# Kernel optimization log

Measured on AMD Instinct MI355X. Metric: run time of the kernel, lower is better.

## Reference

```python
import jax, jax.numpy as jnp
import numpy as np

N_NODES = 100000
N_EDGES = 1600000
IN_DIM = 128
HID_DIM = 128
OUT_DIM = 64
NUM_GRAPHS = 64


def setup_inputs() -> dict:
    key = jax.random.key(0)
    k = jax.random.split(key, 8)
    x = jax.random.normal(k[0], (N_NODES, IN_DIM), dtype=jnp.float32)
    edge_index = jax.random.randint(k[1], (2, N_EDGES), 0, N_NODES, dtype=jnp.int64)
    batch = jnp.sort(jax.random.randint(k[2], (N_NODES,), 0, NUM_GRAPHS, dtype=jnp.int64))
    # glorot-ish init for GCN weights, zero bias (PyG default)
    W1 = jax.random.normal(k[3], (IN_DIM, HID_DIM), dtype=jnp.float32) / np.sqrt(IN_DIM)
    b1 = jnp.zeros((HID_DIM,), dtype=jnp.float32)
    W2 = jax.random.normal(k[4], (HID_DIM, OUT_DIM), dtype=jnp.float32) / np.sqrt(HID_DIM)
    b2 = jnp.zeros((OUT_DIM,), dtype=jnp.float32)
    return {"x": x, "edge_index": edge_index, "batch": batch,
            "W1": W1, "b1": b1, "W2": W2, "b2": b2}


def _gcn_conv(x, W, b, src, dst, norm, n_nodes):
    # x' = scatter_add_{dst}(norm * (xW)[src]) + b   (self-loops already in src/dst)
    h = x @ W                              # [N, D_out]
    msg = norm[:, None] * h[src]           # [E+N, D_out] gather + scale
    out = jax.ops.segment_sum(msg, dst, num_segments=n_nodes)
    return out + b


def _gcn_norm(src, dst, n_nodes):
    # symmetric normalization with self-loops: deg^-1/2[src] * deg^-1/2[dst]
    deg = jax.ops.segment_sum(jnp.ones_like(dst, dtype=jnp.float32), dst,
                              num_segments=n_nodes)
    dinv = jnp.where(deg > 0, jax.lax.rsqrt(deg), 0.0)
    return dinv[src] * dinv[dst]


def reference(x, edge_index, batch, W1, b1, W2, b2):
    n = x.shape[0]
    loops = jnp.arange(n, dtype=edge_index.dtype)
    src = jnp.concatenate([edge_index[0], loops])
    dst = jnp.concatenate([edge_index[1], loops])
    norm = _gcn_norm(src, dst, n)

    h = jax.nn.relu(_gcn_conv(x, W1, b1, src, dst, norm, n))
    h = jax.nn.relu(_gcn_conv(h, W2, b2, src, dst, norm, n))

    # global mean pool per graph
    sums = jax.ops.segment_sum(h, batch, num_segments=NUM_GRAPHS)
    cnts = jax.ops.segment_sum(jnp.ones((n,), dtype=h.dtype), batch,
                               num_segments=NUM_GRAPHS)
    return sums / jnp.maximum(cnts, 1.0)[:, None]
```

## Files before the change

kernel.cpp:

```cpp
#include <hip/hip_runtime.h>

typedef unsigned short ushort_t;
typedef unsigned int uint_t;
typedef __attribute__((ext_vector_type(8))) short bf16x8;
typedef __attribute__((ext_vector_type(4))) float f32x4;

__device__ inline ushort_t bf16_rne(float f) {
    uint_t u = __float_as_uint(f);
    return (ushort_t)((u + 0x7FFFu + ((u >> 16) & 1u)) >> 16);
}

__device__ inline uint_t pack2(float lo, float hi) {
    return (uint_t)bf16_rne(lo) | ((uint_t)bf16_rne(hi) << 16);
}

__device__ inline void acc8(uint4 v, float* a) {
    a[0] += __uint_as_float(v.x << 16);
    a[1] += __uint_as_float(v.x & 0xFFFF0000u);
    a[2] += __uint_as_float(v.y << 16);
    a[3] += __uint_as_float(v.y & 0xFFFF0000u);
    a[4] += __uint_as_float(v.z << 16);
    a[5] += __uint_as_float(v.z & 0xFFFF0000u);
    a[6] += __uint_as_float(v.w << 16);
    a[7] += __uint_as_float(v.w & 0xFFFF0000u);
}

__device__ inline void set8(uint4 v, float* a) {
    a[0] = __uint_as_float(v.x << 16);
    a[1] = __uint_as_float(v.x & 0xFFFF0000u);
    a[2] = __uint_as_float(v.y << 16);
    a[3] = __uint_as_float(v.y & 0xFFFF0000u);
    a[4] = __uint_as_float(v.z << 16);
    a[5] = __uint_as_float(v.z & 0xFFFF0000u);
    a[6] = __uint_as_float(v.w << 16);
    a[7] = __uint_as_float(v.w & 0xFFFF0000u);
}


#define BSH 8
#define NBMAX 512
#define EPB 4096

__global__ __launch_bounds__(256) void k_bhist(const int* __restrict__ dst,
                                               int* __restrict__ bcnt, int E, int nb) {
    __shared__ int h[NBMAX];
    const int tid = threadIdx.x;
    for (int i = tid; i < NBMAX; i += 256) h[i] = 0;
    __syncthreads();
    const int e0 = blockIdx.x * EPB;
    for (int i = tid; i < EPB; i += 256) {
        int e = e0 + i;
        if (e < E) atomicAdd(&h[dst[e] >> BSH], 1);
    }
    __syncthreads();
    for (int i = tid; i < nb; i += 256)
        if (h[i]) atomicAdd(&bcnt[i], h[i]);
}

__global__ __launch_bounds__(512) void k_bscan(const int* __restrict__ bcnt,
                                               int* __restrict__ boff,
                                               int* __restrict__ bcur, int nb) {
    __shared__ int a[NBMAX];
    const int t = threadIdx.x;
    int v = (t < nb) ? bcnt[t] : 0;
    a[t] = v;
    __syncthreads();
    for (int off = 1; off < NBMAX; off <<= 1) {
        int x = (t >= off) ? a[t - off] : 0;
        __syncthreads();
        a[t] += x;
        __syncthreads();
    }
    if (t < nb) {
        int excl = a[t] - v;
        boff[t] = excl;
        bcur[t] = excl;
    }
}

__global__ __launch_bounds__(256) void k_bscatter(const int* __restrict__ src,
                                                  const int* __restrict__ dst,
                                                  int* __restrict__ bcur,
                                                  uint_t* __restrict__ pairs, int E, int nb) {
    __shared__ int h[NBMAX];
    __shared__ int base[NBMAX];
    const int tid = threadIdx.x;
    for (int i = tid; i < NBMAX; i += 256) h[i] = 0;
    __syncthreads();
    const int e0 = blockIdx.x * EPB;
    for (int i = tid; i < EPB; i += 256) {
        int e = e0 + i;
        if (e < E) atomicAdd(&h[dst[e] >> BSH], 1);
    }
    __syncthreads();
    for (int b = tid; b < nb; b += 256) {
        int c = h[b];
        base[b] = c ? atomicAdd(&bcur[b], c) : 0;
        h[b] = 0;
    }
    __syncthreads();
    for (int i = tid; i < EPB; i += 256) {
        int e = e0 + i;
        if (e < E) {
            int s = src[e], d = dst[e];
            int bk = d >> BSH;
            int off = atomicAdd(&h[bk], 1);
            pairs[base[bk] + off] = (uint_t)s | ((uint_t)(d & 255) << 24);
        }
    }
}

__global__ __launch_bounds__(256) void k_bcsr(const uint_t* __restrict__ pairs,
                                              const int* __restrict__ boff,
                                              const int* __restrict__ bcurEnd,
                                              int* __restrict__ rowptr,
                                              int* __restrict__ rowend,
                                              float* __restrict__ dinv,
                                              int* __restrict__ csr, int n) {
    __shared__ int deg[256], sc[256], cur[256];
    const int t = threadIdx.x;
    const int b = blockIdx.x;
    const int beg = boff[b], end = bcurEnd[b];
    deg[t] = 0;
    __syncthreads();
    for (int i = beg + t; i < end; i += 256) {
        uint_t p = pairs[i];
        atomicAdd(&deg[p >> 24], 1);
    }
    __syncthreads();
    int dv = deg[t];
    sc[t] = dv;
    __syncthreads();
    for (int off = 1; off < 256; off <<= 1) {
        int x = (t >= off) ? sc[t - off] : 0;
        __syncthreads();
        sc[t] += x;
        __syncthreads();
    }
    int excl = sc[t] - dv;
    cur[t] = excl;
    int d = (b << BSH) + t;
    if (d < n) {
        int r = beg + excl;
        rowptr[d] = r;
        rowend[d] = r + dv;
        dinv[d] = rsqrtf((float)dv + 1.0f);
    }
    __syncthreads();
    for (int i = beg + t; i < end; i += 256) {
        uint_t p = pairs[i];
        int off = atomicAdd(&cur[p >> 24], 1);
        csr[beg + off] = (int)(p & 0xFFFFFFu);
    }
}


__global__ __launch_bounds__(256) void k_prep_w(const float* __restrict__ W1,
                                                const float* __restrict__ W2,
                                                ushort_t* __restrict__ Wt1,
                                                ushort_t* __restrict__ Wt2) {
    int idx = blockIdx.x * 256 + threadIdx.x;
    if (idx < 16384) {
        int k = idx >> 7, c = idx & 127;
        Wt1[c * 128 + k] = bf16_rne(W1[idx]);
    } else if (idx < 24576) {
        int j = idx - 16384;
        int k = j >> 6, c = j & 63;
        Wt2[c * 128 + k] = bf16_rne(W2[j]);
    }
}


template <int DOUT, bool IN_BF16>
__global__ __launch_bounds__(256) void k_gemm_mfma(const void* __restrict__ Xv,
                                                   const ushort_t* __restrict__ Wt,
                                                   const float* __restrict__ dinv,
                                                   ushort_t* __restrict__ G, int n) {
    constexpr int KP = 136;
    constexpr int NW = DOUT / 2;
    constexpr int NT = NW / 16;
    __shared__ ushort_t Xs[128 * KP];
    __shared__ ushort_t Ws[DOUT * KP];

    const int tid = threadIdx.x;
    const int row0 = blockIdx.x * 128;

    if (!IN_BF16) {
        const float* X = (const float*)Xv;
#pragma unroll
        for (int i = 0; i < 16; i++) {
            int idx = tid * 4 + i * 1024;
            int r = idx >> 7, k = idx & 127;
            int gr = row0 + r;
            float4 v = make_float4(0.f, 0.f, 0.f, 0.f);
            if (gr < n) v = *(const float4*)&X[(size_t)gr * 128 + k];
            ushort4 o;
            o.x = bf16_rne(v.x); o.y = bf16_rne(v.y);
            o.z = bf16_rne(v.z); o.w = bf16_rne(v.w);
            *(ushort4*)&Xs[r * KP + k] = o;
        }
    } else {
        const ushort_t* X = (const ushort_t*)Xv;
#pragma unroll
        for (int i = 0; i < 8; i++) {
            int idx = tid * 8 + i * 2048;
            int r = idx >> 7, k = idx & 127;
            int gr = row0 + r;
            uint4 v = make_uint4(0u, 0u, 0u, 0u);
            if (gr < n) v = *(const uint4*)&X[(size_t)gr * 128 + k];
            *(uint4*)&Xs[r * KP + k] = v;
        }
    }
    constexpr int WI = (DOUT * 128) / 2048;
#pragma unroll
    for (int i = 0; i < WI; i++) {
        int idx = tid * 8 + i * 2048;
        int r = idx >> 7, k = idx & 127;
        *(uint4*)&Ws[r * KP + k] = *(const uint4*)&Wt[idx];
    }
    __syncthreads();

    const int lane = tid & 63;
    const int wid = tid >> 6;
    const int wm = wid & 1, wn = wid >> 1;
    const int lr = lane & 15, kg = lane >> 4;

    f32x4 acc[4][NT];
#pragma unroll
    for (int mi = 0; mi < 4; mi++)
#pragma unroll
        for (int ni = 0; ni < NT; ni++)
#pragma unroll
            for (int q = 0; q < 4; q++) acc[mi][ni][q] = 0.f;

    const ushort_t* xb = &Xs[(wm * 64 + lr) * KP + kg * 8];
    const ushort_t* wb = &Ws[(wn * NW + lr) * KP + kg * 8];

#pragma unroll
    for (int ks = 0; ks < 4; ks++) {
        bf16x8 a[4], b[NT];
#pragma unroll
        for (int mi = 0; mi < 4; mi++)
            a[mi] = *(const bf16x8*)&xb[mi * 16 * KP + ks * 32];
#pragma unroll
        for (int ni = 0; ni < NT; ni++)
            b[ni] = *(const bf16x8*)&wb[ni * 16 * KP + ks * 32];
#pragma unroll
        for (int mi = 0; mi < 4; mi++)
#pragma unroll
            for (int ni = 0; ni < NT; ni++)
                acc[mi][ni] = __builtin_amdgcn_mfma_f32_16x16x32_bf16(
                    a[mi], b[ni], acc[mi][ni], 0, 0, 0);
    }

#pragma unroll
    for (int mi = 0; mi < 4; mi++) {
        int r0 = row0 + wm * 64 + mi * 16 + kg * 4;
#pragma unroll
        for (int r = 0; r < 4; r++) {
            int gr = r0 + r;
            if (gr < n) {
                float s = dinv[gr];
#pragma unroll
                for (int ni = 0; ni < NT; ni++) {
                    int c = wn * NW + ni * 16 + lr;
                    G[(size_t)gr * DOUT + c] = bf16_rne(s * acc[mi][ni][r]);
                }
            }
        }
    }
}


__global__ __launch_bounds__(256) void k_gather128(const int* __restrict__ rowptr,
                                                   const int* __restrict__ rowend,
                                                   const int* __restrict__ csr,
                                                   const ushort_t* __restrict__ G,
                                                   const float* __restrict__ dinv,
                                                   const float* __restrict__ b,
                                                   ushort_t* __restrict__ H, int n) {
    const int g = blockIdx.x * 16 + (threadIdx.x >> 4);
    const int lane = threadIdx.x & 15;
    const int koff = lane * 8;
    if (g >= n) return;
    const int beg = rowptr[g], end = rowend[g];

    float a[8];
    set8(*(const uint4*)&G[(size_t)g * 128 + koff], a);
    int e = beg;
    for (; e + 7 < end; e += 8) {
        int s[8];
#pragma unroll
        for (int j = 0; j < 8; j++) s[j] = csr[e + j];
        uint4 v[8];
#pragma unroll
        for (int j = 0; j < 8; j++)
            v[j] = *(const uint4*)&G[(size_t)s[j] * 128 + koff];
#pragma unroll
        for (int j = 0; j < 8; j++) acc8(v[j], a);
    }
    for (; e + 1 < end; e += 2) {
        int s0 = csr[e], s1 = csr[e + 1];
        uint4 v0 = *(const uint4*)&G[(size_t)s0 * 128 + koff];
        uint4 v1 = *(const uint4*)&G[(size_t)s1 * 128 + koff];
        acc8(v0, a); acc8(v1, a);
    }
    if (e < end) {
        int s0 = csr[e];
        acc8(*(const uint4*)&G[(size_t)s0 * 128 + koff], a);
    }
    const float di = dinv[g];
    float4 bb0 = *(const float4*)&b[koff];
    float4 bb1 = *(const float4*)&b[koff + 4];
    uint4 ov;
    ov.x = pack2(fmaxf(di * a[0] + bb0.x, 0.f), fmaxf(di * a[1] + bb0.y, 0.f));
    ov.y = pack2(fmaxf(di * a[2] + bb0.z, 0.f), fmaxf(di * a[3] + bb0.w, 0.f));
    ov.z = pack2(fmaxf(di * a[4] + bb1.x, 0.f), fmaxf(di * a[5] + bb1.y, 0.f));
    ov.w = pack2(fmaxf(di * a[6] + bb1.z, 0.f), fmaxf(di * a[7] + bb1.w, 0.f));
    *(uint4*)&H[(size_t)g * 128 + koff] = ov;
}


__global__ __launch_bounds__(256) void k_gather64_pool(const int* __restrict__ rowptr,
                                                       const int* __restrict__ rowend,
                                                       const int* __restrict__ csr,
                                                       const ushort_t* __restrict__ G,
                                                       const float* __restrict__ dinv,
                                                       const float* __restrict__ b,
                                                       const int* __restrict__ batch,
                                                       float* __restrict__ pool, int n) {
    __shared__ float po[32][72];
    __shared__ int pg[32];
    const int grp = threadIdx.x >> 3;
    const int lane = threadIdx.x & 7;
    const int g = blockIdx.x * 32 + grp;
    const int koff = lane * 8;

    float o8[8] = {0.f, 0.f, 0.f, 0.f, 0.f, 0.f, 0.f, 0.f};
    if (g < n) {
        float a[8];
        set8(*(const uint4*)&G[(size_t)g * 64 + koff], a);
        int e = rowptr[g];
        const int end = rowend[g];
        for (; e + 7 < end; e += 8) {
            int s[8];
#pragma unroll
            for (int j = 0; j < 8; j++) s[j] = csr[e + j];
            uint4 v[8];
#pragma unroll
            for (int j = 0; j < 8; j++)
                v[j] = *(const uint4*)&G[(size_t)s[j] * 64 + koff];
#pragma unroll
            for (int j = 0; j < 8; j++) acc8(v[j], a);
        }
        for (; e + 1 < end; e += 2) {
            int s0 = csr[e], s1 = csr[e + 1];
            uint4 v0 = *(const uint4*)&G[(size_t)s0 * 64 + koff];
            uint4 v1 = *(const uint4*)&G[(size_t)s1 * 64 + koff];
            acc8(v0, a); acc8(v1, a);
        }
        if (e < end) {
            int s0 = csr[e];
            acc8(*(const uint4*)&G[(size_t)s0 * 64 + koff], a);
        }
        const float di = dinv[g];
        float4 bb0 = *(const float4*)&b[koff];
        float4 bb1 = *(const float4*)&b[koff + 4];
        o8[0] = fmaxf(di * a[0] + bb0.x, 0.f);
        o8[1] = fmaxf(di * a[1] + bb0.y, 0.f);
        o8[2] = fmaxf(di * a[2] + bb0.z, 0.f);
        o8[3] = fmaxf(di * a[3] + bb0.w, 0.f);
        o8[4] = fmaxf(di * a[4] + bb1.x, 0.f);
        o8[5] = fmaxf(di * a[5] + bb1.y, 0.f);
        o8[6] = fmaxf(di * a[6] + bb1.z, 0.f);
        o8[7] = fmaxf(di * a[7] + bb1.w, 0.f);
    }
    if (lane == 0) pg[grp] = (g < n) ? batch[g] : -1;
    *(float4*)&po[grp][koff] = make_float4(o8[0], o8[1], o8[2], o8[3]);
    *(float4*)&po[grp][koff + 4] = make_float4(o8[4], o8[5], o8[6], o8[7]);
    __syncthreads();

    if (threadIdx.x < 64) {
        const int c = threadIdx.x;
        float run = 0.f;
        int cur = -1;
        for (int r = 0; r < 32; r++) {
            int gr = pg[r];
            if (gr < 0) continue;
            if (gr != cur) {
                if (cur >= 0) atomicAdd(&pool[cur * 64 + c], run);
                cur = gr;
                run = 0.f;
            }
            run += po[r][c];
        }
        if (cur >= 0) atomicAdd(&pool[cur * 64 + c], run);
    }
}


__global__ __launch_bounds__(64) void k_div_bs(const float* __restrict__ pool,
                                               const int* __restrict__ batch,
                                               float* __restrict__ out, int n) {
    int t = blockIdx.x * 64 + threadIdx.x;
    int g = t >> 6;
    int lo = 0, hi = n;
    while (lo < hi) { int m = (lo + hi) >> 1; if (batch[m] < g) lo = m + 1; else hi = m; }
    int lb = lo;
    lo = lb; hi = n;
    while (lo < hi) { int m = (lo + hi) >> 1; if (batch[m] <= g) lo = m + 1; else hi = m; }
    float c = (float)(lo - lb);
    c = c > 1.f ? c : 1.f;
    out[t] = pool[t] / c;
}


extern "C" void kernel_launch(void* const* d_in, const int* in_sizes, int n_in,
                              void* d_out, int out_size, void* d_ws, size_t ws_size,
                              hipStream_t stream) {
    const float* x = (const float*)d_in[0];
    const int* edge = (const int*)d_in[1];
    const int* batch = (const int*)d_in[2];
    const float* W1 = (const float*)d_in[3];
    const float* b1 = (const float*)d_in[4];
    const float* W2 = (const float*)d_in[5];
    const float* b2 = (const float*)d_in[6];

    const int n = in_sizes[0] / 128;
    const int E = in_sizes[1] / 2;
    const int* src = edge;
    const int* dst = edge + E;
    const int nb = (n + 255) >> BSH;

    size_t nA = ((size_t)n + 255) & ~(size_t)255;
    float* dinv = (float*)d_ws;
    int* rowptr = (int*)(dinv + nA);
    int* rowend = rowptr + nA;
    int* bcnt = rowend + nA;
    int* boff = bcnt + NBMAX;
    int* bcur = boff + NBMAX;
    float* pool = (float*)(bcur + NBMAX);
    ushort_t* Wt1 = (ushort_t*)(pool + 4096 + 256);
    ushort_t* Wt2 = Wt1 + 16384;
    ushort_t* bufG = Wt2 + 8192;
    ushort_t* bufH = bufG + (size_t)n * 128;
    int* csr = (int*)(bufH + (size_t)n * 128);
    uint_t* pairs = (uint_t*)bufG;

    hipMemsetAsync(bcnt, 0, NBMAX * 4, stream);
    hipMemsetAsync(pool, 0, 4096 * 4, stream);

    k_prep_w<<<96, 256, 0, stream>>>(W1, W2, Wt1, Wt2);

    int gE = (E + EPB - 1) / EPB;
    k_bhist<<<gE, 256, 0, stream>>>(dst, bcnt, E, nb);
    k_bscan<<<1, NBMAX, 0, stream>>>(bcnt, boff, bcur, nb);
    k_bscatter<<<gE, 256, 0, stream>>>(src, dst, bcur, pairs, E, nb);
    k_bcsr<<<nb, 256, 0, stream>>>(pairs, boff, bcur, rowptr, rowend, dinv, csr, n);

    k_gemm_mfma<128, false><<<(n + 127) / 128, 256, 0, stream>>>(x, Wt1, dinv, bufG, n);
    k_gather128<<<(n + 15) / 16, 256, 0, stream>>>(rowptr, rowend, csr, bufG, dinv, b1,
                                                   bufH, n);

    k_gemm_mfma<64, true><<<(n + 127) / 128, 256, 0, stream>>>(bufH, Wt2, dinv, bufG, n);
    k_gather64_pool<<<(n + 31) / 32, 256, 0, stream>>>(rowptr, rowend, csr, bufG, dinv,
                                                       b2, batch, pool, n);

    k_div_bs<<<64, 64, 0, stream>>>(pool, batch, (float*)d_out, n);
}
```

Before: 211.1 us.

## Store per-block histograms to skip re-histogramming in scatter, merge weight prep

Result: slower. 287.4 us (+36.1%).

```diff
diff --git a/kernel.cpp b/kernel.cpp
--- a/kernel.cpp
+++ b/kernel.cpp
@@ -41,86 +41,100 @@
 #define NBMAX 512
 #define EPB 4096
 
-__global__ __launch_bounds__(256) void k_bhist(const int* __restrict__ dst,
-                                               int* __restrict__ bcnt, int E, int nb) {
+__global__ __launch_bounds__(256) void k_bhist_prep(const int* __restrict__ dst,
+                                                    int* __restrict__ blockhist,
+                                                    const float* __restrict__ W1,
+                                                    const float* __restrict__ W2,
+                                                    ushort_t* __restrict__ Wt1,
+                                                    ushort_t* __restrict__ Wt2,
+                                                    int E, int nb, int gE) {
+    const int b = blockIdx.x;
+    const int tid = threadIdx.x;
+    if (b >= gE) {
+        int idx = (b - gE) * 256 + tid;
+        if (idx < 16384) {
+            int k = idx >> 7, c = idx & 127;
+            Wt1[c * 128 + k] = bf16_rne(W1[idx]);
+        } else if (idx < 24576) {
+            int j = idx - 16384;
+            int k = j >> 6, c = j & 63;
+            Wt2[c * 128 + k] = bf16_rne(W2[j]);
+        }
+        return;
+    }
     __shared__ int h[NBMAX];
-    const int tid = threadIdx.x;
     for (int i = tid; i < NBMAX; i += 256) h[i] = 0;
     __syncthreads();
-    const int e0 = blockIdx.x * EPB;
+    const int e0 = b * EPB;
     for (int i = tid; i < EPB; i += 256) {
         int e = e0 + i;
         if (e < E) atomicAdd(&h[dst[e] >> BSH], 1);
     }
     __syncthreads();
-    for (int i = tid; i < nb; i += 256)
-        if (h[i]) atomicAdd(&bcnt[i], h[i]);
-}
-
-__global__ __launch_bounds__(512) void k_bscan(const int* __restrict__ bcnt,
-                                               int* __restrict__ boff,
-                                               int* __restrict__ bcur, int nb) {
+    for (int i = tid; i < nb; i += 256) blockhist[b * NBMAX + i] = h[i];
+}
+
+__global__ __launch_bounds__(512) void k_bscan2(int* __restrict__ blockhist,
+                                                int* __restrict__ boff,
+                                                int* __restrict__ bend,
+                                                int* __restrict__ rowptr,
+                                                int nBlk, int nb, int n, int E) {
     __shared__ int a[NBMAX];
-    const int t = threadIdx.x;
-    int v = (t < nb) ? bcnt[t] : 0;
-    a[t] = v;
+    const int k = threadIdx.x;
+    int total = 0;
+    if (k < nb)
+        for (int b = 0; b < nBlk; b++) total += blockhist[b * NBMAX + k];
+    a[k] = total;
     __syncthreads();
     for (int off = 1; off < NBMAX; off <<= 1) {
-        int x = (t >= off) ? a[t - off] : 0;
+        int x = (k >= off) ? a[k - off] : 0;
         __syncthreads();
-        a[t] += x;
+        a[k] += x;
         __syncthreads();
     }
-    if (t < nb) {
-        int excl = a[t] - v;
-        boff[t] = excl;
-        bcur[t] = excl;
-    }
+    if (k < nb) {
+        int excl = a[k] - total;
+        boff[k] = excl;
+        bend[k] = excl + total;
+        int run = excl;
+        for (int b = 0; b < nBlk; b++) {
+            int t = blockhist[b * NBMAX + k];
+            blockhist[b * NBMAX + k] = run;
+            run += t;
+        }
+    }
+    if (k == 0) rowptr[n] = E;
 }
 
 __global__ __launch_bounds__(256) void k_bscatter(const int* __restrict__ src,
                                                   const int* __restrict__ dst,
-                                                  int* __restrict__ bcur,
+                                                  const int* __restrict__ blockhist,
                                                   uint_t* __restrict__ pairs, int E, int nb) {
-    __shared__ int h[NBMAX];
-    __shared__ int base[NBMAX];
+    __shared__ int cur[NBMAX];
     const int tid = threadIdx.x;
-    for (int i = tid; i < NBMAX; i += 256) h[i] = 0;
+    for (int i = tid; i < nb; i += 256) cur[i] = blockhist[blockIdx.x * NBMAX + i];
     __syncthreads();
     const int e0 = blockIdx.x * EPB;
-    for (int i = tid; i < EPB; i += 256) {
-        int e = e0 + i;
-        if (e < E) atomicAdd(&h[dst[e] >> BSH], 1);
-    }
-    __syncthreads();
-    for (int b = tid; b < nb; b += 256) {
-        int c = h[b];
-        base[b] = c ? atomicAdd(&bcur[b], c) : 0;
-        h[b] = 0;
-    }
-    __syncthreads();
     for (int i = tid; i < EPB; i += 256) {
         int e = e0 + i;
         if (e < E) {
             int s = src[e], d = dst[e];
-            int bk = d >> BSH;
-            int off = atomicAdd(&h[bk], 1);
-            pairs[base[bk] + off] = (uint_t)s | ((uint_t)(d & 255) << 24);
+            int off = atomicAdd(&cur[d >> BSH], 1);
+            pairs[off] = (uint_t)s | ((uint_t)(d & 255) << 24);
         }
     }
 }
 
 __global__ __launch_bounds__(256) void k_bcsr(const uint_t* __restrict__ pairs,
                                               const int* __restrict__ boff,
-                                              const int* __restrict__ bcurEnd,
+                                              const int* __restrict__ bend,
                                               int* __restrict__ rowptr,
-                                              int* __restrict__ rowend,
                                               float* __restrict__ dinv,
                                               int* __restrict__ csr, int n) {
     __shared__ int deg[256], sc[256], cur[256];
     const int t = threadIdx.x;
     const int b = blockIdx.x;
-    const int beg = boff[b], end = bcurEnd[b];
+    const int beg = boff[b], end = bend[b];
     deg[t] = 0;
     __syncthreads();
     for (int i = beg + t; i < end; i += 256) {
@@ -141,9 +155,7 @@
     cur[t] = excl;
     int d = (b << BSH) + t;
     if (d < n) {
-        int r = beg + excl;
-        rowptr[d] = r;
-        rowend[d] = r + dv;
+        rowptr[d] = beg + excl;
         dinv[d] = rsqrtf((float)dv + 1.0f);
     }
     __syncthreads();
@@ -151,22 +163,6 @@
         uint_t p = pairs[i];
         int off = atomicAdd(&cur[p >> 24], 1);
         csr[beg + off] = (int)(p & 0xFFFFFFu);
-    }
-}
-
-
-__global__ __launch_bounds__(256) void k_prep_w(const float* __restrict__ W1,
-                                                const float* __restrict__ W2,
-                                                ushort_t* __restrict__ Wt1,
-                                                ushort_t* __restrict__ Wt2) {
-    int idx = blockIdx.x * 256 + threadIdx.x;
-    if (idx < 16384) {
-        int k = idx >> 7, c = idx & 127;
-        Wt1[c * 128 + k] = bf16_rne(W1[idx]);
-    } else if (idx < 24576) {
-        int j = idx - 16384;
-        int k = j >> 6, c = j & 63;
-        Wt2[c * 128 + k] = bf16_rne(W2[j]);
     }
 }
 
@@ -273,7 +269,6 @@
 
 
 __global__ __launch_bounds__(256) void k_gather128(const int* __restrict__ rowptr,
-                                                   const int* __restrict__ rowend,
                                                    const int* __restrict__ csr,
                                                    const ushort_t* __restrict__ G,
                                                    const float* __restrict__ dinv,
@@ -283,7 +278,7 @@
     const int lane = threadIdx.x & 15;
     const int koff = lane * 8;
     if (g >= n) return;
-    const int beg = rowptr[g], end = rowend[g];
+    const int beg = rowptr[g], end = rowptr[g + 1];
 
     float a[8];
     set8(*(const uint4*)&G[(size_t)g * 128 + koff], a);
@@ -322,7 +317,6 @@
 
 
 __global__ __launch_bounds__(256) void k_gather64_pool(const int* __restrict__ rowptr,
-                                                       const int* __restrict__ rowend,
                                                        const int* __restrict__ csr,
                                                        const ushort_t* __restrict__ G,
                                                        const float* __restrict__ dinv,
@@ -341,7 +335,7 @@
         float a[8];
         set8(*(const uint4*)&G[(size_t)g * 64 + koff], a);
         int e = rowptr[g];
-        const int end = rowend[g];
+        const int end = rowptr[g + 1];
         for (; e + 7 < end; e += 8) {
             int s[8];
 #pragma unroll
@@ -431,40 +425,36 @@
     const int* src = edge;
     const int* dst = edge + E;
     const int nb = (n + 255) >> BSH;
-
-    size_t nA = ((size_t)n + 255) & ~(size_t)255;
+    const int gE = (E + EPB - 1) / EPB;
+
+    size_t nA = ((size_t)n + 256) & ~(size_t)255;
     float* dinv = (float*)d_ws;
     int* rowptr = (int*)(dinv + nA);
-    int* rowend = rowptr + nA;
-    int* bcnt = rowend + nA;
-    int* boff = bcnt + NBMAX;
-    int* bcur = boff + NBMAX;
-    float* pool = (float*)(bcur + NBMAX);
+    int* boff = rowptr + nA;
+    int* bend = boff + NBMAX;
+    float* pool = (float*)(bend + NBMAX);
     ushort_t* Wt1 = (ushort_t*)(pool + 4096 + 256);
     ushort_t* Wt2 = Wt1 + 16384;
     ushort_t* bufG = Wt2 + 8192;
     ushort_t* bufH = bufG + (size_t)n * 128;
     int* csr = (int*)(bufH + (size_t)n * 128);
     uint_t* pairs = (uint_t*)bufG;
-
-    hipMemsetAsync(bcnt, 0, NBMAX * 4, stream);
+    int* blockhist = (int*)(pairs + E);
+
     hipMemsetAsync(pool, 0, 4096 * 4, stream);
 
-    k_prep_w<<<96, 256, 0, stream>>>(W1, W2, Wt1, Wt2);
-
-    int gE = (E + EPB - 1) / EPB;
-    k_bhist<<<gE, 256, 0, stream>>>(dst, bcnt, E, nb);
-    k_bscan<<<1, NBMAX, 0, stream>>>(bcnt, boff, bcur, nb);
-    k_bscatter<<<gE, 256, 0, stream>>>(src, dst, bcur, pairs, E, nb);
-    k_bcsr<<<nb, 256, 0, stream>>>(pairs, boff, bcur, rowptr, rowend, dinv, csr, n);
+    k_bhist_prep<<<gE + 96, 256, 0, stream>>>(dst, blockhist, W1, W2, Wt1, Wt2,
+                                              E, nb, gE);
+    k_bscan2<<<1, NBMAX, 0, stream>>>(blockhist, boff, bend, rowptr, gE, nb, n, E);
+    k_bscatter<<<gE, 256, 0, stream>>>(src, dst, blockhist, pairs, E, nb);
+    k_bcsr<<<nb, 256, 0, stream>>>(pairs, boff, bend, rowptr, dinv, csr, n);
 
     k_gemm_mfma<128, false><<<(n + 127) / 128, 256, 0, stream>>>(x, Wt1, dinv, bufG, n);
-    k_gather128<<<(n + 15) / 16, 256, 0, stream>>>(rowptr, rowend, csr, bufG, dinv, b1,
-                                                   bufH, n);
+    k_gather128<<<(n + 15) / 16, 256, 0, stream>>>(rowptr, csr, bufG, dinv, b1, bufH, n);
 
     k_gemm_mfma<64, true><<<(n + 127) / 128, 256, 0, stream>>>(bufH, Wt2, dinv, bufG, n);
-    k_gather64_pool<<<(n + 31) / 32, 256, 0, stream>>>(rowptr, rowend, csr, bufG, dinv,
-                                                       b2, batch, pool, n);
+    k_gather64_pool<<<(n + 31) / 32, 256, 0, stream>>>(rowptr, csr, bufG, dinv, b2,
+                                                       batch, pool, n);
 
     k_div_bs<<<64, 64, 0, stream>>>(pool, batch, (float*)d_out, n);
 }
```
